# Optimization experiments

Measured on AMD Instinct MI355X. Metric: run time of the kernel, lower is better.

The kernel has to match this reference:

```python
import jax, jax.numpy as jnp
import numpy as np

HIDDEN = 2048
NUM_HEADS = 16
HEAD_DIM = HIDDEN // NUM_HEADS
ROPE_THETA = 10000.0


def _rope_cos_sin(n, dtype):
    # Llama-style: inv_freq over even indices, emb = concat([freqs, freqs])
    inv_freq = 1.0 / (ROPE_THETA ** (jnp.arange(0, HEAD_DIM, 2, dtype=jnp.float32) / HEAD_DIM))
    pos = jnp.arange(n, dtype=jnp.float32)
    freqs = pos[:, None] * inv_freq[None, :]          # [N, HEAD_DIM/2]
    emb = jnp.concatenate([freqs, freqs], axis=-1)    # [N, HEAD_DIM]
    return jnp.cos(emb).astype(dtype), jnp.sin(emb).astype(dtype)


def _rotate_half(x):
    x1, x2 = jnp.split(x, 2, axis=-1)
    return jnp.concatenate([-x2, x1], axis=-1)


def setup_inputs() -> dict:
    key = jax.random.key(0)
    ks = jax.random.split(key, 5)
    B, N, D = 2, 2048, HIDDEN
    s = 1.0 / np.sqrt(D)
    return {
        "x": jax.random.normal(ks[0], (B, N, D), jnp.float32),
        "Wq": jax.random.normal(ks[1], (D, D), jnp.float32) * s,
        "Wk": jax.random.normal(ks[2], (D, D), jnp.float32) * s,
        "Wv": jax.random.normal(ks[3], (D, D), jnp.float32) * s,
        "Wo": jax.random.normal(ks[4], (D, D), jnp.float32) * s,
    }


def reference(x, Wq, Wk, Wv, Wo):
    B, N, D = x.shape
    scale = HEAD_DIM ** -0.5

    def proj(W):  # nn.Linear(bias=False): x @ W.T, then split heads -> [B,H,N,hd]
        return (x @ W.T).reshape(B, N, NUM_HEADS, HEAD_DIM).transpose(0, 2, 1, 3)

    q, k, v = proj(Wq), proj(Wk), proj(Wv)

    cos, sin = _rope_cos_sin(N, x.dtype)  # [N, HEAD_DIM]
    cos = cos[None, None]                 # broadcast over B, H
    sin = sin[None, None]
    q = q * cos + _rotate_half(q) * sin
    k = k * cos + _rotate_half(k) * sin

    attn = jnp.einsum("bhqd,bhkd->bhqk", q, k) * scale  # full N x N scores
    attn = jax.nn.softmax(attn, axis=-1)                 # dropout p=0 -> identity
    out = jnp.einsum("bhqk,bhkd->bhqd", attn, v)
    out = out.transpose(0, 2, 1, 3).reshape(B, N, D)
    return out @ Wo.T
```

## Files before the change

kernel.cpp:

```cpp
#include <hip/hip_runtime.h>
#include <hip/hip_bf16.h>
#include <math.h>

typedef short bf16x8 __attribute__((ext_vector_type(8)));
typedef short bf16x4 __attribute__((ext_vector_type(4)));
typedef float f32x4 __attribute__((ext_vector_type(4)));

#define NSEQ 2048
#define DMODEL 2048
#define NH 16
#define HD 128
#define BATCH 2
#define MROWS 4096

__device__ __forceinline__ unsigned short f2b(float f) {
    __hip_bfloat16 h = __float2bfloat16(f);
    return *reinterpret_cast<unsigned short*>(&h);
}
__device__ __forceinline__ float b2f(unsigned short u) {
    __hip_bfloat16 h;
    *reinterpret_cast<unsigned short*>(&h) = u;
    return __bfloat162float(h);
}

__device__ __forceinline__ void gld_lds16(const unsigned short* g, unsigned short* l) {
    __builtin_amdgcn_global_load_lds(
        (const __attribute__((address_space(1))) unsigned int*)(const void*)g,
        (__attribute__((address_space(3))) unsigned int*)(void*)l,
        16, 0, 0);
}

__global__ __launch_bounds__(256) void cast_all_kernel(const float* __restrict__ x,
                                                       const float* __restrict__ wq,
                                                       const float* __restrict__ wk,
                                                       const float* __restrict__ wv,
                                                       const float* __restrict__ wo,
                                                       unsigned short* __restrict__ xb,
                                                       unsigned short* __restrict__ wqb) {
    int bid = blockIdx.x;
    const float* src;
    unsigned short* dst;
    int off;
    if (bid < 4096) {
        src = x; dst = xb; off = bid;
    } else {
        int w = (bid - 4096) >> 11;
        src = (w == 0) ? wq : (w == 1) ? wk : (w == 2) ? wv : wo;
        dst = wqb + (size_t)w * 4194304;
        off = (bid - 4096) & 2047;
    }
    int i = (off * 256 + threadIdx.x) * 8;
    float4 a = *(const float4*)(src + i);
    float4 b = *(const float4*)(src + i + 4);
    union { unsigned short u[8]; uint4 v; } tmp;
    tmp.u[0] = f2b(a.x); tmp.u[1] = f2b(a.y); tmp.u[2] = f2b(a.z); tmp.u[3] = f2b(a.w);
    tmp.u[4] = f2b(b.x); tmp.u[5] = f2b(b.y); tmp.u[6] = f2b(b.z); tmp.u[7] = f2b(b.w);
    *(uint4*)(dst + i) = tmp.v;
}

__global__ __launch_bounds__(256) void gemm_qkv(const unsigned short* __restrict__ A,
                                                const unsigned short* __restrict__ Bw,
                                                unsigned short* __restrict__ qk,
                                                unsigned short* __restrict__ vt) {
    __shared__ unsigned short sA[128 * 32];
    __shared__ unsigned short sB[128 * 32];
    const int K = DMODEL;
    const int tid = threadIdx.x;
    const int wave = tid >> 6, lane = tid & 63;
    const int m0 = blockIdx.y * 128, n0 = blockIdx.x * 128;
    const int wm = wave * 32;

    f32x4 acc[2][8] = {};

    const int srow = wave * 32 + (lane >> 2);
    const int scol = (lane & 3) * 8;
    const unsigned short* Ag = A + (size_t)(m0 + srow) * K + scol;
    const unsigned short* Bg = Bw + (size_t)(n0 + srow) * K + scol;
    unsigned short* sA0 = &sA[(wave * 32) * 32];
    unsigned short* sA1 = &sA[(wave * 32 + 16) * 32];
    unsigned short* sB0 = &sB[(wave * 32) * 32];
    unsigned short* sB1 = &sB[(wave * 32 + 16) * 32];
    const int fr = lane & 15, fo = (lane >> 4) * 8;

    for (int kb = 0; kb < K; kb += 32) {
        gld_lds16(Ag + kb, sA0);
        gld_lds16(Ag + (size_t)16 * K + kb, sA1);
        gld_lds16(Bg + kb, sB0);
        gld_lds16(Bg + (size_t)16 * K + kb, sB1);
        __syncthreads();
        bf16x8 af[2], bfr[8];
        #pragma unroll
        for (int mt = 0; mt < 2; mt++)
            af[mt] = *(const bf16x8*)&sA[(wm + mt * 16 + fr) * 32 + fo];
        #pragma unroll
        for (int nt = 0; nt < 8; nt++)
            bfr[nt] = *(const bf16x8*)&sB[(nt * 16 + fr) * 32 + fo];
        #pragma unroll
        for (int mt = 0; mt < 2; mt++)
            #pragma unroll
            for (int nt = 0; nt < 8; nt++)
                acc[mt][nt] = __builtin_amdgcn_mfma_f32_16x16x32_bf16(af[mt], bfr[nt], acc[mt][nt], 0, 0, 0);
        __syncthreads();
    }

    const int g4 = (lane >> 4) * 4, c0 = lane & 15;
    if (n0 < 4096) {
        const float scale = (n0 < 2048) ? 0.08838834764831845f : 1.0f;
        unsigned short* dst = qk + (size_t)(n0 >> 11) * 8388608;
        const int colbase = n0 & 2047;
        float invf[4];
        #pragma unroll
        for (int nt = 0; nt < 4; nt++)
            invf[nt] = exp2f((float)(nt * 16 + c0) * -0.2076205059304545f);
        #pragma unroll
        for (int mt = 0; mt < 2; mt++) {
            #pragma unroll
            for (int r = 0; r < 4; r++) {
                int row = m0 + wm + mt * 16 + g4 + r;
                float nf = (float)(row & (NSEQ - 1));
                size_t rbase = (size_t)row * 2048 + colbase + c0;
                #pragma unroll
                for (int nt = 0; nt < 4; nt++) {
                    float sv, cv;
                    __sincosf(nf * invf[nt], &sv, &cv);
                    float lo = acc[mt][nt][r], hi = acc[mt][nt + 4][r];
                    dst[rbase + nt * 16]      = f2b((lo * cv - hi * sv) * scale);
                    dst[rbase + nt * 16 + 64] = f2b((hi * cv + lo * sv) * scale);
                }
            }
        }
    } else {
        #pragma unroll
        for (int mt = 0; mt < 2; mt++) {
            int mbase = m0 + wm + mt * 16 + g4;
            int bb = mbase >> 11;
            int nn = mbase & 2047;
            #pragma unroll
            for (int nt = 0; nt < 8; nt++) {
                int d = n0 - 4096 + nt * 16 + c0;
                union { unsigned short u[4]; uint2 v; } o;
                #pragma unroll
                for (int r = 0; r < 4; r++) o.u[r] = f2b(acc[mt][nt][r]);
                *(uint2*)(vt + ((size_t)(bb * 2048 + d)) * 2048 + nn) = o.v;
            }
        }
    }
}

__global__ __launch_bounds__(256) void gemm_out(const unsigned short* __restrict__ A,
                                                const unsigned short* __restrict__ Bw,
                                                float* __restrict__ Cf) {
    __shared__ unsigned short sA[128 * 64];
    __shared__ unsigned short sB[128 * 64];
    const int K = DMODEL, Nn = DMODEL;
    const int tid = threadIdx.x;
    const int wave = tid >> 6, lane = tid & 63;
    const int m0 = blockIdx.y * 128, n0 = blockIdx.x * 128;
    const int wm = (wave >> 1) * 64, wn = (wave & 1) * 64;

    f32x4 acc[4][4] = {};

    const int srowoff = wave * 8 + (lane >> 3);
    const int gchunk = ((lane & 7) ^ ((lane >> 3) & 7)) * 8;
    const unsigned short* Ag = A + (size_t)(m0 + srowoff) * K + gchunk;
    const unsigned short* Bg = Bw + (size_t)(n0 + srowoff) * K + gchunk;
    unsigned short* sAw = &sA[(wave * 8) * 64];
    unsigned short* sBw = &sB[(wave * 8) * 64];

    const int fr = lane & 15, grp = lane >> 4;
    const int swz = fr & 7;

    for (int kb = 0; kb < K; kb += 64) {
        #pragma unroll
        for (int i = 0; i < 4; i++)
            gld_lds16(Ag + (size_t)(i * 32) * K + kb, sAw + i * 32 * 64);
        #pragma unroll
        for (int i = 0; i < 4; i++)
            gld_lds16(Bg + (size_t)(i * 32) * K + kb, sBw + i * 32 * 64);
        __syncthreads();
        #pragma unroll
        for (int ks = 0; ks < 2; ks++) {
            bf16x8 af[4], bfr[4];
            #pragma unroll
            for (int mt = 0; mt < 4; mt++)
                af[mt] = *(const bf16x8*)&sA[(wm + mt * 16 + fr) * 64 + (((ks * 4 + grp) ^ swz) << 3)];
            #pragma unroll
            for (int nt = 0; nt < 4; nt++)
                bfr[nt] = *(const bf16x8*)&sB[(wn + nt * 16 + fr) * 64 + (((ks * 4 + grp) ^ swz) << 3)];
            #pragma unroll
            for (int mt = 0; mt < 4; mt++)
                #pragma unroll
                for (int nt = 0; nt < 4; nt++)
                    acc[mt][nt] = __builtin_amdgcn_mfma_f32_16x16x32_bf16(af[mt], bfr[nt], acc[mt][nt], 0, 0, 0);
        }
        __syncthreads();
    }

    const int g4 = (lane >> 4) * 4, c0 = lane & 15;
    #pragma unroll
    for (int mt = 0; mt < 4; mt++)
        #pragma unroll
        for (int nt = 0; nt < 4; nt++) {
            int col = n0 + wn + nt * 16 + c0;
            #pragma unroll
            for (int r = 0; r < 4; r++) {
                int row = m0 + wm + mt * 16 + g4 + r;
                Cf[(size_t)row * Nn + col] = acc[mt][nt][r];
            }
        }
}

__global__ __launch_bounds__(256) void attn_kernel(const unsigned short* __restrict__ Q,
                                                   const unsigned short* __restrict__ Kg,
                                                   const unsigned short* __restrict__ Vt,
                                                   unsigned short* __restrict__ O) {
    __shared__ unsigned short sK[64 * 136];
    __shared__ unsigned short sV[128 * 88];

    const int bh = blockIdx.x;
    const int b = bh >> 4, h = bh & 15;
    const int qt = blockIdx.y;
    const int tid = threadIdx.x, wave = tid >> 6, lane = tid & 63;
    const int c0 = lane & 15, grp = lane >> 4;

    bf16x8 qf[2][4];
    {
        const unsigned short* Qbase = Q + (size_t)(b * NSEQ + qt * 128 + wave * 32 + c0) * DMODEL + h * HD + grp * 8;
        #pragma unroll
        for (int nt = 0; nt < 2; nt++)
            #pragma unroll
            for (int ks = 0; ks < 4; ks++)
                qf[nt][ks] = *(const bf16x8*)(Qbase + (size_t)nt * 16 * DMODEL + ks * 32);
    }

    f32x4 oacc[8][2] = {};
    float lsum[2] = {0.f, 0.f};

    const unsigned short* Kbase = Kg + (size_t)(b * NSEQ) * DMODEL + h * HD;
    const unsigned short* Vbase = Vt + (size_t)(bh * HD) * NSEQ;

    for (int kv0 = 0; kv0 < NSEQ; kv0 += 64) {
        __syncthreads();
        #pragma unroll
        for (int i = 0; i < 4; i++) {
            int fl = i * 256 + tid;
            int rr = fl >> 4, cc = fl & 15;
            *(uint4*)&sK[rr * 136 + cc * 8] = *(const uint4*)(Kbase + (size_t)(kv0 + rr) * DMODEL + cc * 8);
        }
        #pragma unroll
        for (int i = 0; i < 4; i++) {
            int fl = i * 256 + tid;
            int rr = fl >> 3, cc = fl & 7;
            *(uint4*)&sV[rr * 88 + cc * 8] = *(const uint4*)(Vbase + (size_t)rr * NSEQ + kv0 + cc * 8);
        }
        __syncthreads();

        f32x4 s[4][2] = {};
        #pragma unroll
        for (int ks = 0; ks < 4; ks++) {
            bf16x8 kf[4];
            #pragma unroll
            for (int mt = 0; mt < 4; mt++)
                kf[mt] = *(const bf16x8*)&sK[(mt * 16 + c0) * 136 + ks * 32 + grp * 8];
            #pragma unroll
            for (int mt = 0; mt < 4; mt++)
                #pragma unroll
                for (int nt = 0; nt < 2; nt++)
                    s[mt][nt] = __builtin_amdgcn_mfma_f32_16x16x32_bf16(kf[mt], qf[nt][ks], s[mt][nt], 0, 0, 0);
        }

        bf16x4 pk[4][2];
        #pragma unroll
        for (int mt = 0; mt < 4; mt++)
            #pragma unroll
            for (int nt = 0; nt < 2; nt++) {
                float p0 = __expf(s[mt][nt][0]);
                float p1 = __expf(s[mt][nt][1]);
                float p2 = __expf(s[mt][nt][2]);
                float p3 = __expf(s[mt][nt][3]);
                lsum[nt] += (p0 + p1) + (p2 + p3);
                bf16x4 t;
                t[0] = (short)f2b(p0); t[1] = (short)f2b(p1);
                t[2] = (short)f2b(p2); t[3] = (short)f2b(p3);
                pk[mt][nt] = t;
            }

        #pragma unroll
        for (int mtK = 0; mtK < 4; mtK++) {
            bf16x4 va[8];
            #pragma unroll
            for (int mo = 0; mo < 8; mo++)
                va[mo] = *(const bf16x4*)&sV[(mo * 16 + c0) * 88 + mtK * 16 + grp * 4];
            #pragma unroll
            for (int mo = 0; mo < 8; mo++)
                #pragma unroll
                for (int nt = 0; nt < 2; nt++)
                    oacc[mo][nt] = __builtin_amdgcn_mfma_f32_16x16x16bf16_1k(va[mo], pk[mtK][nt], oacc[mo][nt], 0, 0, 0);
        }
    }

    float invl[2];
    #pragma unroll
    for (int nt = 0; nt < 2; nt++) {
        float li = lsum[nt];
        li += __shfl_xor(li, 16);
        li += __shfl_xor(li, 32);
        invl[nt] = 1.0f / li;
    }
    #pragma unroll
    for (int mo = 0; mo < 8; mo++)
        #pragma unroll
        for (int nt = 0; nt < 2; nt++) {
            union { unsigned short u[4]; uint2 v; } o;
            #pragma unroll
            for (int r = 0; r < 4; r++)
                o.u[r] = f2b(oacc[mo][nt][r] * invl[nt]);
            int row = b * NSEQ + qt * 128 + wave * 32 + nt * 16 + c0;
            int col = h * HD + mo * 16 + grp * 4;
            *(uint2*)(O + (size_t)row * DMODEL + col) = o.v;
        }
}

extern "C" void kernel_launch(void* const* d_in, const int* in_sizes, int n_in,
                              void* d_out, int out_size, void* d_ws, size_t ws_size,
                              hipStream_t stream) {
    const float* x  = (const float*)d_in[0];
    const float* Wq = (const float*)d_in[1];
    const float* Wk = (const float*)d_in[2];
    const float* Wv = (const float*)d_in[3];
    const float* Wo = (const float*)d_in[4];

    char* ws = (char*)d_ws;
    unsigned short* xb  = (unsigned short*)(ws);
    unsigned short* wqb = (unsigned short*)(ws + 16777216);
    unsigned short* wob = (unsigned short*)(ws + 16777216 + 3 * 8388608);
    unsigned short* qb  = (unsigned short*)(ws + 50331648);
    unsigned short* kb  = (unsigned short*)(ws + 67108864);
    unsigned short* vt  = (unsigned short*)(ws + 83886080);

    cast_all_kernel<<<12288, 256, 0, stream>>>(x, Wq, Wk, Wv, Wo, xb, wqb);

    gemm_qkv<<<dim3(48, 32), 256, 0, stream>>>(xb, wqb, qb, vt);

    attn_kernel<<<dim3(32, 16), 256, 0, stream>>>(qb, kb, vt, xb);

    gemm_out<<<dim3(16, 32), 256, 0, stream>>>(xb, wob, (float*)d_out);
}
```

Measured before the change: 388.8 us.

## Widen QKV GEMM K-tile to 64 and XOR-swizzle LDS layout

```diff
diff --git a/kernel.cpp b/kernel.cpp
--- a/kernel.cpp
+++ b/kernel.cpp
@@ -62,8 +62,8 @@
                                                 const unsigned short* __restrict__ Bw,
                                                 unsigned short* __restrict__ qk,
                                                 unsigned short* __restrict__ vt) {
-    __shared__ unsigned short sA[128 * 32];
-    __shared__ unsigned short sB[128 * 32];
+    __shared__ unsigned short sA[128 * 64];
+    __shared__ unsigned short sB[128 * 64];
     const int K = DMODEL;
     const int tid = threadIdx.x;
     const int wave = tid >> 6, lane = tid & 63;
@@ -72,34 +72,39 @@
 
     f32x4 acc[2][8] = {};
 
-    const int srow = wave * 32 + (lane >> 2);
-    const int scol = (lane & 3) * 8;
-    const unsigned short* Ag = A + (size_t)(m0 + srow) * K + scol;
-    const unsigned short* Bg = Bw + (size_t)(n0 + srow) * K + scol;
-    unsigned short* sA0 = &sA[(wave * 32) * 32];
-    unsigned short* sA1 = &sA[(wave * 32 + 16) * 32];
-    unsigned short* sB0 = &sB[(wave * 32) * 32];
-    unsigned short* sB1 = &sB[(wave * 32 + 16) * 32];
-    const int fr = lane & 15, fo = (lane >> 4) * 8;
-
-    for (int kb = 0; kb < K; kb += 32) {
-        gld_lds16(Ag + kb, sA0);
-        gld_lds16(Ag + (size_t)16 * K + kb, sA1);
-        gld_lds16(Bg + kb, sB0);
-        gld_lds16(Bg + (size_t)16 * K + kb, sB1);
-        __syncthreads();
-        bf16x8 af[2], bfr[8];
-        #pragma unroll
-        for (int mt = 0; mt < 2; mt++)
-            af[mt] = *(const bf16x8*)&sA[(wm + mt * 16 + fr) * 32 + fo];
-        #pragma unroll
-        for (int nt = 0; nt < 8; nt++)
-            bfr[nt] = *(const bf16x8*)&sB[(nt * 16 + fr) * 32 + fo];
-        #pragma unroll
-        for (int mt = 0; mt < 2; mt++)
+    const int srowoff = wave * 8 + (lane >> 3);
+    const int gchunk = ((lane & 7) ^ ((lane >> 3) & 7)) * 8;
+    const unsigned short* Ag = A + (size_t)(m0 + srowoff) * K + gchunk;
+    const unsigned short* Bg = Bw + (size_t)(n0 + srowoff) * K + gchunk;
+    unsigned short* sAw = &sA[(wave * 8) * 64];
+    unsigned short* sBw = &sB[(wave * 8) * 64];
+
+    const int fr = lane & 15, grp = lane >> 4;
+    const int swz = fr & 7;
+
+    for (int kb = 0; kb < K; kb += 64) {
+        #pragma unroll
+        for (int i = 0; i < 4; i++)
+            gld_lds16(Ag + (size_t)(i * 32) * K + kb, sAw + i * 32 * 64);
+        #pragma unroll
+        for (int i = 0; i < 4; i++)
+            gld_lds16(Bg + (size_t)(i * 32) * K + kb, sBw + i * 32 * 64);
+        __syncthreads();
+        #pragma unroll
+        for (int ks = 0; ks < 2; ks++) {
+            bf16x8 af[2], bfr[8];
+            #pragma unroll
+            for (int mt = 0; mt < 2; mt++)
+                af[mt] = *(const bf16x8*)&sA[(wm + mt * 16 + fr) * 64 + (((ks * 4 + grp) ^ swz) << 3)];
             #pragma unroll
             for (int nt = 0; nt < 8; nt++)
-                acc[mt][nt] = __builtin_amdgcn_mfma_f32_16x16x32_bf16(af[mt], bfr[nt], acc[mt][nt], 0, 0, 0);
+                bfr[nt] = *(const bf16x8*)&sB[(nt * 16 + fr) * 64 + (((ks * 4 + grp) ^ swz) << 3)];
+            #pragma unroll
+            for (int mt = 0; mt < 2; mt++)
+                #pragma unroll
+                for (int nt = 0; nt < 8; nt++)
+                    acc[mt][nt] = __builtin_amdgcn_mfma_f32_16x16x32_bf16(af[mt], bfr[nt], acc[mt][nt], 0, 0, 0);
+        }
         __syncthreads();
     }
 
```

Measured after the change: 396.7 us. 1.02x slower.
